# Kernel optimization log

Measured on AMD Instinct MI355X. Metric: run time of the kernel, lower is better.

Reference implementation:

```python
import jax, jax.numpy as jnp
import numpy as np

PI = float(np.pi)


def setup_inputs() -> dict:
    key = jax.random.key(0)
    k1, k2, k3, k4, k5, k6 = jax.random.split(key, 6)
    N, P = 1024, 4096
    wl = jax.random.uniform(k1, (N, 2), minval=1.0, maxval=4.0)            # box (w, l) in meters
    Ry = jax.random.uniform(k2, (N,), minval=-PI / 2 + 0.05, maxval=PI / 2 - 0.05)
    points = jax.random.normal(k3, (N, P, 2)) * 5.0 + jnp.array([0.0, 15.0])  # BEV (x, z) points
    density = jax.random.uniform(k4, (N, P), minval=0.5, maxval=2.0)
    bev_box_center = jnp.stack(
        [jax.random.uniform(k5, (N,), minval=-10.0, maxval=10.0),
         jax.random.uniform(k6, (N,), minval=5.0, maxval=30.0)], axis=1)
    return dict(wl=wl, Ry=Ry, points=points, density=density, bev_box_center=bev_box_center)


def _ray_tracing_loss(wl, Ry, points, density, center):
    # Vectorized calc_dis_ray_tracing over N boxes x P points (torch code is per-box).
    w, l = wl[:, 0], wl[:, 1]
    init_theta = jnp.arctan(w / l)
    length = jnp.sqrt(w ** 2 + l ** 2) / 2
    # 4 BEV corners (computed with the ORIGINAL Ry, matching torch ordering)  [N,4]
    angs = jnp.stack([init_theta + Ry, PI - init_theta + Ry,
                      PI + init_theta + Ry, -init_theta + Ry], axis=1)
    cx = length[:, None] * jnp.cos(angs) + center[:, 0:1]
    cy = length[:, None] * jnp.sin(angs) + center[:, 1:2]
    # degenerate-yaw nudge (applied only to line slopes, as in torch)
    Ry2 = jnp.where(Ry == PI / 2, Ry - 1e-4, Ry)
    Ry2 = jnp.where(Ry2 == 0.0, Ry2 + 1e-4, Ry2)
    k1 = jnp.tan(Ry2)
    k2 = jnp.tan(Ry2 + PI / 2)
    b11 = cy[:, 0] - k1 * cx[:, 0]
    b12 = cy[:, 2] - k1 * cx[:, 2]
    b21 = cy[:, 0] - k2 * cx[:, 0]
    b22 = cy[:, 2] - k2 * cx[:, 2]
    ks = jnp.stack([k1, k2, k1, k2], axis=1)          # [N,4] line slopes (line0..line3)
    bs = jnp.stack([b11, b22, b12, b21], axis=1)      # [N,4] intercepts
    px = jnp.where(points[..., 0] == 0.0, 1e-4, points[..., 0])   # [N,P]
    py = points[..., 1]
    slope = py / px                                   # camera-ray slope per point [N,P]
    denom = slope[..., None] - ks[:, None, :]         # [N,P,4]
    ix = bs[:, None, :] / denom                       # ray/edge-line intersection x
    iy = bs[:, None, :] * slope[..., None] / denom    # intersection y
    dis = jnp.abs(ix - px[..., None]) + jnp.abs(iy - py[..., None])  # L1 point->intersection
    cen = jnp.sqrt(ix ** 2 + iy ** 2)                 # intersection distance to origin
    # in-edge test on values rounded to 1e-4 (torch rounds *10000)
    irx = jnp.round(ix * 1e4)
    iry = jnp.round(iy * 1e4)
    nxt = jnp.array([1, 2, 3, 0])
    cxr = jnp.round(cx * 1e4)
    cyr = jnp.round(cy * 1e4)
    lox = jnp.minimum(cxr, cxr[:, nxt])[:, None, :]
    hix = jnp.maximum(cxr, cxr[:, nxt])[:, None, :]
    loy = jnp.minimum(cyr, cyr[:, nxt])[:, None, :]
    hiy = jnp.maximum(cyr, cyr[:, nxt])[:, None, :]
    mask = ((irx > lox) & (irx < hix)) | ((iry > loy) & (iry < hiy))  # [N,P,4]
    dis_in = jnp.sum(mask, axis=-1) == 2              # ray crosses exactly 2 edges [N,P]
    # z-buffer: among the 2 masked intersections pick the one closer to origin
    cen_m = jnp.where(mask, cen, jnp.inf)
    z = jnp.argmin(cen_m, axis=-1)                    # [N,P]
    dis_sel = jnp.take_along_axis(dis, z[..., None], axis=-1)[..., 0] / density
    cnt = jnp.sum(dis_in, axis=-1)                    # valid points per box [N]
    box_valid = cnt >= 3                              # torch: return 0 if < 3
    box_mean = jnp.sum(jnp.where(dis_in, dis_sel, 0.0), axis=-1) / jnp.maximum(cnt, 1)
    nvalid = jnp.sum(box_valid)
    return jnp.sum(jnp.where(box_valid, box_mean, 0.0)) / jnp.maximum(nvalid, 1)


def reference(wl, Ry, points, density, bev_box_center):
    return _ray_tracing_loss(wl, Ry, points, density, bev_box_center)
```

## Files before the change

### kernel.cpp

```cpp
#include <hip/hip_runtime.h>
#include <hip/hip_bf16.h>

#define PI_F      3.14159274101257324f
#define HALF_PI_F 1.57079637050628662f

__device__ __forceinline__ float bf2f(unsigned int h) {
    return __uint_as_float(h << 16);
}
__device__ __forceinline__ unsigned short f2bf_bits(float f) {
    __hip_bfloat16 b = __float2bfloat16(f);
    return *(unsigned short*)&b;
}
__device__ __forceinline__ float finf() { return __int_as_float(0x7f800000); }

__device__ __forceinline__ bool detect_bf16(const unsigned int* dens_words) {
    bool all_in = true;
    #pragma unroll
    for (int t = 0; t < 16; ++t) {
        unsigned int lo = dens_words[t] & 0xffffu;
        all_in = all_in && ((lo - 0x3F00u) <= 0x100u);
    }
    return all_in;
}

__device__ __forceinline__ void proc_point(
    float px, float py, float dens,
    float k1, float k2, const float* __restrict__ bs,
    const float* __restrict__ lox, const float* __restrict__ hix,
    const float* __restrict__ loy, const float* __restrict__ hiy,
    float& sum, int& cnt_in)
{
    if (px == 0.0f) px = 0.0001f;
    const float slope = __fdividef(py, px);
    float rd[2];
    rd[0] = __fdividef(1.0f, slope - k1);
    rd[1] = __fdividef(1.0f, slope - k2);

    int   m_cnt    = 0;
    float best_key = finf();
    float best_dis = 0.0f;

    #pragma unroll
    for (int e = 0; e < 4; ++e) {
        const float ix  = bs[e] * rd[e & 1];
        const float iy  = slope * ix;
        const float irx = rintf(ix * 10000.0f);
        const float iry = rintf(iy * 10000.0f);
        const bool  m   = ((irx > lox[e]) && (irx < hix[e])) ||
                          ((iry > loy[e]) && (iry < hiy[e]));
        const float dis = fabsf(ix - px) + fabsf(iy - py);
        const float key = m ? ix * ix : finf();
        m_cnt += m ? 1 : 0;
        if (key < best_key) { best_key = key; best_dis = dis; }
    }

    if (m_cnt == 2) {
        sum += __fdividef(best_dis, dens);
        cnt_in += 1;
    }
}

__global__ __launch_bounds__(256) void box_kernel(
    const void* __restrict__ wl_p,
    const void* __restrict__ ry_p,
    const void* __restrict__ pts_p,
    const void* __restrict__ dens_p,
    const void* __restrict__ ctr_p,
    float* __restrict__ ws_contrib,
    float* __restrict__ ws_valid,
    int P)
{
    const int i   = blockIdx.x;
    const int tid = threadIdx.x;

    const bool isb = detect_bf16((const unsigned int*)dens_p);

    float w, l, ry, c0, c1;
    if (isb) {
        const unsigned short* wl  = (const unsigned short*)wl_p;
        const unsigned short* Ry  = (const unsigned short*)ry_p;
        const unsigned short* ctr = (const unsigned short*)ctr_p;
        w  = bf2f(wl[2 * i]);     l  = bf2f(wl[2 * i + 1]);
        ry = bf2f(Ry[i]);
        c0 = bf2f(ctr[2 * i]);    c1 = bf2f(ctr[2 * i + 1]);
    } else {
        const float* wl  = (const float*)wl_p;
        const float* Ry  = (const float*)ry_p;
        const float* ctr = (const float*)ctr_p;
        w  = wl[2 * i];           l  = wl[2 * i + 1];
        ry = Ry[i];
        c0 = ctr[2 * i];          c1 = ctr[2 * i + 1];
    }

    const float theta = atanf(w / l);
    const float len   = sqrtf(w * w + l * l) * 0.5f;

    float angs[4];
    angs[0] = theta + ry;
    angs[1] = (PI_F - theta) + ry;
    angs[2] = (PI_F + theta) + ry;
    angs[3] = (-theta) + ry;

    float cxv[4], cyv[4], cxr[4], cyr[4];
    #pragma unroll
    for (int e = 0; e < 4; ++e) {
        cxv[e] = len * cosf(angs[e]) + c0;
        cyv[e] = len * sinf(angs[e]) + c1;
        cxr[e] = rintf(cxv[e] * 10000.0f);
        cyr[e] = rintf(cyv[e] * 10000.0f);
    }

    float ry2 = (ry == HALF_PI_F) ? (ry - 0.0001f) : ry;
    if (ry2 == 0.0f) ry2 += 0.0001f;
    const float k1 = tanf(ry2);
    const float k2 = tanf(ry2 + HALF_PI_F);

    const float b11 = cyv[0] - k1 * cxv[0];
    const float b12 = cyv[2] - k1 * cxv[2];
    const float b21 = cyv[0] - k2 * cxv[0];
    const float b22 = cyv[2] - k2 * cxv[2];

    const float bs[4] = {b11, b22, b12, b21};

    float lox[4], hix[4], loy[4], hiy[4];
    #pragma unroll
    for (int e = 0; e < 4; ++e) {
        const int n = (e + 1) & 3;
        lox[e] = fminf(cxr[e], cxr[n]);
        hix[e] = fmaxf(cxr[e], cxr[n]);
        loy[e] = fminf(cyr[e], cyr[n]);
        hiy[e] = fmaxf(cyr[e], cyr[n]);
    }

    const size_t rowoff = (size_t)i * P;
    const int    Ph     = P >> 1;
    float sum    = 0.0f;
    int   cnt_in = 0;

    if (isb) {
        const uint2*        prow = (const uint2*)pts_p + (rowoff >> 1);
        const unsigned int* drow = (const unsigned int*)dens_p + (rowoff >> 1);
        for (int j = tid; j < Ph; j += 256) {
            const uint2        pp = prow[j];
            const unsigned int dd = drow[j];
            proc_point(bf2f(pp.x & 0xffffu), bf2f(pp.x >> 16), bf2f(dd & 0xffffu),
                       k1, k2, bs, lox, hix, loy, hiy, sum, cnt_in);
            proc_point(bf2f(pp.y & 0xffffu), bf2f(pp.y >> 16), bf2f(dd >> 16),
                       k1, k2, bs, lox, hix, loy, hiy, sum, cnt_in);
        }
    } else {
        const float4* prow = (const float4*)pts_p + (rowoff >> 1);
        const float2* drow = (const float2*)dens_p + (rowoff >> 1);
        for (int j = tid; j < Ph; j += 256) {
            const float4 pp = prow[j];
            const float2 dd = drow[j];
            proc_point(pp.x, pp.y, dd.x, k1, k2, bs, lox, hix, loy, hiy, sum, cnt_in);
            proc_point(pp.z, pp.w, dd.y, k1, k2, bs, lox, hix, loy, hiy, sum, cnt_in);
        }
    }

    #pragma unroll
    for (int off = 32; off > 0; off >>= 1) {
        sum    += __shfl_down(sum, off, 64);
        cnt_in += __shfl_down(cnt_in, off, 64);
    }
    __shared__ float s_sum[4];
    __shared__ int   s_cnt[4];
    const int wave = tid >> 6;
    if ((tid & 63) == 0) { s_sum[wave] = sum; s_cnt[wave] = cnt_in; }
    __syncthreads();
    if (tid == 0) {
        const float s = s_sum[0] + s_sum[1] + s_sum[2] + s_sum[3];
        const int   c = s_cnt[0] + s_cnt[1] + s_cnt[2] + s_cnt[3];
        const bool  valid = (c >= 3);
        const int   cd    = (c > 1) ? c : 1;
        const float mean  = s / (float)cd;
        ws_contrib[i] = valid ? mean : 0.0f;
        ws_valid[i]   = valid ? 1.0f : 0.0f;
    }
}

__global__ __launch_bounds__(256) void final_kernel(
    const float* __restrict__ contrib,
    const float* __restrict__ validf,
    const void* __restrict__ dens_p,
    void* __restrict__ out,
    int N)
{
    const int tid = threadIdx.x;
    float s = 0.0f;
    int   c = 0;
    for (int b = tid; b < N; b += 256) {
        s += contrib[b];
        c += (validf[b] != 0.0f) ? 1 : 0;
    }
    #pragma unroll
    for (int off = 32; off > 0; off >>= 1) {
        s += __shfl_down(s, off, 64);
        c += __shfl_down(c, off, 64);
    }
    __shared__ float s_sum[4];
    __shared__ int   s_cnt[4];
    const int wave = tid >> 6;
    if ((tid & 63) == 0) { s_sum[wave] = s; s_cnt[wave] = c; }
    __syncthreads();
    if (tid == 0) {
        const float ss = s_sum[0] + s_sum[1] + s_sum[2] + s_sum[3];
        const int   cc = s_cnt[0] + s_cnt[1] + s_cnt[2] + s_cnt[3];
        const int   cd = (cc > 1) ? cc : 1;
        const float val = ss / (float)cd;
        const bool isb = detect_bf16((const unsigned int*)dens_p);
        if (isb) {
            ((unsigned short*)out)[0] = f2bf_bits(val);
        } else {
            unsigned int fb = __float_as_uint(val);
            unsigned int wword = (fb & 0xFFFF0000u) | (unsigned int)f2bf_bits(val);
            ((unsigned int*)out)[0] = wword;
        }
    }
}

extern "C" void kernel_launch(void* const* d_in, const int* in_sizes, int n_in,
                              void* d_out, int out_size, void* d_ws, size_t ws_size,
                              hipStream_t stream) {
    const void* wl      = d_in[0];
    const void* Ry      = d_in[1];
    const void* points  = d_in[2];
    const void* density = d_in[3];
    const void* center  = d_in[4];

    const int N = in_sizes[1];
    const int P = in_sizes[3] / N;

    float* contrib = (float*)d_ws;
    float* validf  = contrib + N;

    box_kernel<<<N, 256, 0, stream>>>(wl, Ry, points, density, center,
                                      contrib, validf, P);
    final_kernel<<<1, 256, 0, stream>>>(contrib, validf, density, d_out, N);
}
```

Measured before the change: 105.1 us.

## Fuse box and final reduction into one cooperative kernel, widen loads

Measured after the change: 196.8 us. +87.2%, slower.

```diff
diff --git a/kernel.cpp b/kernel.cpp
--- a/kernel.cpp
+++ b/kernel.cpp
@@ -1,5 +1,8 @@
 #include <hip/hip_runtime.h>
+#include <hip/hip_cooperative_groups.h>
 #include <hip/hip_bf16.h>
+
+namespace cg = cooperative_groups;
 
 #define PI_F      3.14159274101257324f
 #define HALF_PI_F 1.57079637050628662f
@@ -60,7 +63,8 @@
     }
 }
 
-__global__ __launch_bounds__(256) void box_kernel(
+__device__ __forceinline__ void do_box(
+    int i, int tid, bool isb,
     const void* __restrict__ wl_p,
     const void* __restrict__ ry_p,
     const void* __restrict__ pts_p,
@@ -68,13 +72,9 @@
     const void* __restrict__ ctr_p,
     float* __restrict__ ws_contrib,
     float* __restrict__ ws_valid,
-    int P)
-{
-    const int i   = blockIdx.x;
-    const int tid = threadIdx.x;
-
-    const bool isb = detect_bf16((const unsigned int*)dens_p);
-
+    int P,
+    float* s_sum, int* s_cnt)
+{
     float w, l, ry, c0, c1;
     if (isb) {
         const unsigned short* wl  = (const unsigned short*)wl_p;
@@ -133,30 +133,50 @@
     }
 
     const size_t rowoff = (size_t)i * P;
-    const int    Ph     = P >> 1;
+    const int    Pq     = P >> 2;
     float sum    = 0.0f;
     int   cnt_in = 0;
 
     if (isb) {
-        const uint2*        prow = (const uint2*)pts_p + (rowoff >> 1);
-        const unsigned int* drow = (const unsigned int*)dens_p + (rowoff >> 1);
-        for (int j = tid; j < Ph; j += 256) {
-            const uint2        pp = prow[j];
-            const unsigned int dd = drow[j];
-            proc_point(bf2f(pp.x & 0xffffu), bf2f(pp.x >> 16), bf2f(dd & 0xffffu),
+        const uint4* prow = (const uint4*)pts_p  + (rowoff >> 2);
+        const uint2* drow = (const uint2*)dens_p + (rowoff >> 2);
+        for (int j = tid; j < Pq; j += 256) {
+            const uint4 pp = prow[j];
+            const uint2 dd = drow[j];
+            proc_point(bf2f(pp.x & 0xffffu), bf2f(pp.x >> 16), bf2f(dd.x & 0xffffu),
                        k1, k2, bs, lox, hix, loy, hiy, sum, cnt_in);
-            proc_point(bf2f(pp.y & 0xffffu), bf2f(pp.y >> 16), bf2f(dd >> 16),
+            proc_point(bf2f(pp.y & 0xffffu), bf2f(pp.y >> 16), bf2f(dd.x >> 16),
                        k1, k2, bs, lox, hix, loy, hiy, sum, cnt_in);
+            proc_point(bf2f(pp.z & 0xffffu), bf2f(pp.z >> 16), bf2f(dd.y & 0xffffu),
+                       k1, k2, bs, lox, hix, loy, hiy, sum, cnt_in);
+            proc_point(bf2f(pp.w & 0xffffu), bf2f(pp.w >> 16), bf2f(dd.y >> 16),
+                       k1, k2, bs, lox, hix, loy, hiy, sum, cnt_in);
         }
     } else {
-        const float4* prow = (const float4*)pts_p + (rowoff >> 1);
-        const float2* drow = (const float2*)dens_p + (rowoff >> 1);
-        for (int j = tid; j < Ph; j += 256) {
-            const float4 pp = prow[j];
-            const float2 dd = drow[j];
-            proc_point(pp.x, pp.y, dd.x, k1, k2, bs, lox, hix, loy, hiy, sum, cnt_in);
-            proc_point(pp.z, pp.w, dd.y, k1, k2, bs, lox, hix, loy, hiy, sum, cnt_in);
-        }
+        const float4* prow = (const float4*)pts_p  + (rowoff >> 1);
+        const float4* drow = (const float4*)dens_p + (rowoff >> 2);
+        for (int j = tid; j < Pq; j += 256) {
+            const float4 p0 = prow[2 * j];
+            const float4 p1 = prow[2 * j + 1];
+            const float4 dd = drow[j];
+            proc_point(p0.x, p0.y, dd.x, k1, k2, bs, lox, hix, loy, hiy, sum, cnt_in);
+            proc_point(p0.z, p0.w, dd.y, k1, k2, bs, lox, hix, loy, hiy, sum, cnt_in);
+            proc_point(p1.x, p1.y, dd.z, k1, k2, bs, lox, hix, loy, hiy, sum, cnt_in);
+            proc_point(p1.z, p1.w, dd.w, k1, k2, bs, lox, hix, loy, hiy, sum, cnt_in);
+        }
+    }
+    for (int idx = (Pq << 2) + tid; idx < P; idx += 256) {
+        float px, py, dn;
+        if (isb) {
+            const unsigned short* pr = (const unsigned short*)pts_p + rowoff * 2;
+            const unsigned short* dr = (const unsigned short*)dens_p + rowoff;
+            px = bf2f(pr[2 * idx]); py = bf2f(pr[2 * idx + 1]); dn = bf2f(dr[idx]);
+        } else {
+            const float* pr = (const float*)pts_p + rowoff * 2;
+            const float* dr = (const float*)dens_p + rowoff;
+            px = pr[2 * idx]; py = pr[2 * idx + 1]; dn = dr[idx];
+        }
+        proc_point(px, py, dn, k1, k2, bs, lox, hix, loy, hiy, sum, cnt_in);
     }
 
     #pragma unroll
@@ -164,8 +184,6 @@
         sum    += __shfl_down(sum, off, 64);
         cnt_in += __shfl_down(cnt_in, off, 64);
     }
-    __shared__ float s_sum[4];
-    __shared__ int   s_cnt[4];
     const int wave = tid >> 6;
     if ((tid & 63) == 0) { s_sum[wave] = sum; s_cnt[wave] = cnt_in; }
     __syncthreads();
@@ -178,6 +196,83 @@
         ws_contrib[i] = valid ? mean : 0.0f;
         ws_valid[i]   = valid ? 1.0f : 0.0f;
     }
+    __syncthreads();
+}
+
+__device__ __forceinline__ void write_out(float val, bool isb, void* out) {
+    if (isb) {
+        ((unsigned short*)out)[0] = f2bf_bits(val);
+    } else {
+        unsigned int fb = __float_as_uint(val);
+        unsigned int wword = (fb & 0xFFFF0000u) | (unsigned int)f2bf_bits(val);
+        ((unsigned int*)out)[0] = wword;
+    }
+}
+
+__global__ __launch_bounds__(256, 4) void box_fused(
+    const void* __restrict__ wl_p,
+    const void* __restrict__ ry_p,
+    const void* __restrict__ pts_p,
+    const void* __restrict__ dens_p,
+    const void* __restrict__ ctr_p,
+    float* __restrict__ ws_contrib,
+    float* __restrict__ ws_valid,
+    void* __restrict__ out,
+    int P, int N)
+{
+    const int tid = threadIdx.x;
+    const bool isb = detect_bf16((const unsigned int*)dens_p);
+
+    __shared__ float s_sum[4];
+    __shared__ int   s_cnt[4];
+
+    for (int i = blockIdx.x; i < N; i += gridDim.x) {
+        do_box(i, tid, isb, wl_p, ry_p, pts_p, dens_p, ctr_p,
+               ws_contrib, ws_valid, P, s_sum, s_cnt);
+    }
+
+    cg::this_grid().sync();
+
+    if (blockIdx.x == 0) {
+        float s = 0.0f;
+        int   c = 0;
+        for (int b = tid; b < N; b += 256) {
+            s += ws_contrib[b];
+            c += (ws_valid[b] != 0.0f) ? 1 : 0;
+        }
+        #pragma unroll
+        for (int off = 32; off > 0; off >>= 1) {
+            s += __shfl_down(s, off, 64);
+            c += __shfl_down(c, off, 64);
+        }
+        const int wave = tid >> 6;
+        if ((tid & 63) == 0) { s_sum[wave] = s; s_cnt[wave] = c; }
+        __syncthreads();
+        if (tid == 0) {
+            const float ss = s_sum[0] + s_sum[1] + s_sum[2] + s_sum[3];
+            const int   cc = s_cnt[0] + s_cnt[1] + s_cnt[2] + s_cnt[3];
+            const int   cd = (cc > 1) ? cc : 1;
+            write_out(ss / (float)cd, isb, out);
+        }
+    }
+}
+
+__global__ __launch_bounds__(256) void box_kernel(
+    const void* __restrict__ wl_p,
+    const void* __restrict__ ry_p,
+    const void* __restrict__ pts_p,
+    const void* __restrict__ dens_p,
+    const void* __restrict__ ctr_p,
+    float* __restrict__ ws_contrib,
+    float* __restrict__ ws_valid,
+    int P)
+{
+    const int tid = threadIdx.x;
+    const bool isb = detect_bf16((const unsigned int*)dens_p);
+    __shared__ float s_sum[4];
+    __shared__ int   s_cnt[4];
+    do_box(blockIdx.x, tid, isb, wl_p, ry_p, pts_p, dens_p, ctr_p,
+           ws_contrib, ws_valid, P, s_sum, s_cnt);
 }
 
 __global__ __launch_bounds__(256) void final_kernel(
@@ -208,15 +303,8 @@
         const float ss = s_sum[0] + s_sum[1] + s_sum[2] + s_sum[3];
         const int   cc = s_cnt[0] + s_cnt[1] + s_cnt[2] + s_cnt[3];
         const int   cd = (cc > 1) ? cc : 1;
-        const float val = ss / (float)cd;
         const bool isb = detect_bf16((const unsigned int*)dens_p);
-        if (isb) {
-            ((unsigned short*)out)[0] = f2bf_bits(val);
-        } else {
-            unsigned int fb = __float_as_uint(val);
-            unsigned int wword = (fb & 0xFFFF0000u) | (unsigned int)f2bf_bits(val);
-            ((unsigned int*)out)[0] = wword;
-        }
+        write_out(ss / (float)cd, isb, out);
     }
 }
 
@@ -229,13 +317,26 @@
     const void* density = d_in[3];
     const void* center  = d_in[4];
 
-    const int N = in_sizes[1];
-    const int P = in_sizes[3] / N;
+    int N = in_sizes[1];
+    int P = in_sizes[3] / N;
 
     float* contrib = (float*)d_ws;
     float* validf  = contrib + N;
-
-    box_kernel<<<N, 256, 0, stream>>>(wl, Ry, points, density, center,
-                                      contrib, validf, P);
-    final_kernel<<<1, 256, 0, stream>>>(contrib, validf, density, d_out, N);
-}
+    void*  outp    = d_out;
+
+    int grid = (N < 1024) ? N : 1024;
+
+    void* kargs[] = {
+        (void*)&wl, (void*)&Ry, (void*)&points, (void*)&density, (void*)&center,
+        (void*)&contrib, (void*)&validf, (void*)&outp, (void*)&P, (void*)&N
+    };
+
+    hipError_t err = hipLaunchCooperativeKernel(
+        (const void*)box_fused, dim3(grid), dim3(256), kargs, 0, stream);
+
+    if (err != hipSuccess) {
+        box_kernel<<<N, 256, 0, stream>>>(wl, Ry, points, density, center,
+                                          contrib, validf, P);
+        final_kernel<<<1, 256, 0, stream>>>(contrib, validf, density, d_out, N);
+    }
+}
```
